# Kernel tuning notes

Measured on AMD Instinct MI355X. Metric: run time of the kernel, lower is better.

The kernel has to match this reference:

```python
import jax, jax.numpy as jnp
import numpy as np

N = 262144
LOC_ENC_LEN = 60
NUM_WEIGHTS = 8
INDIM = 32
OUTDIM = 32
HIDDEN = 32
NEG_SLOPE = 0.01  # nn.LeakyReLU default


def _linear_init(key, fan_in, fan_out):
    # torch nn.Linear default: U(-1/sqrt(fan_in), 1/sqrt(fan_in))
    kw, kb = jax.random.split(key)
    bound = 1.0 / np.sqrt(fan_in)
    w = jax.random.uniform(kw, (fan_in, fan_out), jnp.float32, -bound, bound)
    b = jax.random.uniform(kb, (fan_out,), jnp.float32, -bound, bound)
    return w, b


def setup_inputs() -> dict:
    key = jax.random.key(0)
    ks = jax.random.split(key, 10)
    rel_loc_feat = jax.random.normal(ks[0], (N, LOC_ENC_LEN), jnp.float32)
    feat = jax.random.normal(ks[1], (N, INDIM), jnp.float32)
    dims = [LOC_ENC_LEN, HIDDEN, HIDDEN, HIDDEN, HIDDEN, HIDDEN, NUM_WEIGHTS]
    params = {}
    for i in range(6):
        w, b = _linear_init(ks[2 + i], dims[i], dims[i + 1])
        params[f'sn_w{i}'] = w
        params[f'sn_b{i}'] = b
    # weights_bank: kaiming_normal on [num_weights, indim*outdim] -> std = sqrt(2/fan_in), fan_in = indim*outdim
    std = np.sqrt(2.0 / (INDIM * OUTDIM))
    params['bank'] = jax.random.normal(ks[9], (NUM_WEIGHTS, INDIM * OUTDIM), jnp.float32) * std
    return {'rel_loc_feat': rel_loc_feat, 'feat': feat, **params}


def _score_net(x, ws, bs):
    # 5 Linear+LeakyReLU blocks, then final Linear (no activation)
    for i in range(5):
        x = x @ ws[i] + bs[i]
        x = jnp.where(x >= 0, x, NEG_SLOPE * x)
    return x @ ws[5] + bs[5]


def reference(rel_loc_feat, feat,
              sn_w0, sn_b0, sn_w1, sn_b1, sn_w2, sn_b2,
              sn_w3, sn_b3, sn_w4, sn_b4, sn_w5, sn_b5, bank):
    ws = [sn_w0, sn_w1, sn_w2, sn_w3, sn_w4, sn_w5]
    bs = [sn_b0, sn_b1, sn_b2, sn_b3, sn_b4, sn_b5]
    logits = _score_net(rel_loc_feat, ws, bs)          # [N, num_weights]
    coeff = jax.nn.softmax(logits, axis=-1)            # [N, num_weights]
    # per-point weight matrix: [N, indim*outdim] -> [N, indim, outdim]
    weights = (coeff @ bank).reshape(coeff.shape[0], INDIM, OUTDIM)
    # per-point matmul: feat[:, None] @ weights -> squeeze
    out = jnp.einsum('ni,nio->no', feat, weights)      # [N, outdim]
    return out
```

## Files before the change

### kernel.cpp

```cpp
#include <hip/hip_runtime.h>
#include <stdint.h>


typedef __attribute__((ext_vector_type(8))) __bf16 bf16x8;
typedef __attribute__((ext_vector_type(2))) __bf16 bf16x2;
typedef __attribute__((ext_vector_type(4))) float f32x4;

union FragU { uint32_t u[4]; bf16x8 v; uint4 q; };

__device__ __forceinline__ unsigned short f2bf(float f) {
    union { float f; uint32_t i; } v; v.f = f;
    return (unsigned short)((v.i + 0x7FFFu + ((v.i >> 16) & 1u)) >> 16);
}
__device__ __forceinline__ float bf2f(uint32_t u16) {
    union { uint32_t i; float f; } v; v.i = u16 << 16; return v.f;
}
__device__ __forceinline__ uint32_t pk2(float x, float y) {
    union { bf16x2 h; uint32_t u; } c;
    c.h[0] = (__bf16)x; c.h[1] = (__bf16)y;
    return c.u;
}
__device__ __forceinline__ bf16x8 pack8(float a, float b, float c, float d,
                                        float e, float f, float g, float h) {
    bf16x8 v;
    v[0] = (__bf16)a; v[1] = (__bf16)b; v[2] = (__bf16)c; v[3] = (__bf16)d;
    v[4] = (__bf16)e; v[5] = (__bf16)f; v[6] = (__bf16)g; v[7] = (__bf16)h;
    return v;
}
__device__ __forceinline__ int permK(int k) {
    return 4 * (k >> 3) + (k & 3) + 16 * ((k >> 2) & 1);
}
__device__ __forceinline__ f32x4 MF(bf16x8 a, bf16x8 b, f32x4 c) {
    return __builtin_amdgcn_mfma_f32_16x16x32_bf16(a, b, c, 0, 0, 0);
}


struct WPf { const float* p[13]; };

__global__ void pc_prep(WPf wp, uint32_t* __restrict__ ws) {
    int idx = blockIdx.x * blockDim.x + threadIdx.x;
    if (idx >= 10240) return;
    if (idx < 7424) {
        int layer, t, chunk = 0, lane, d; const float* w; bool perm;
        int r = idx;
        if (r < 1024) { chunk = r >> 9; r &= 511; t = r >> 8; r &= 255; lane = r >> 2; d = r & 3;
                        layer = 0; w = wp.p[0]; perm = false; }
        else if (r < 3072) { r -= 1024; layer = 1 + (r >> 9); r &= 511; t = r >> 8; r &= 255;
                             lane = r >> 2; d = r & 3; w = wp.p[2 * layer]; perm = true; }
        else if (r < 3328) { r -= 3072; layer = 5; t = 0; lane = r >> 2; d = r & 3;
                             w = wp.p[10]; perm = true; }
        else { r -= 3328; int bk = r >> 9; r &= 511; t = r >> 8; r &= 255; lane = r >> 2; d = r & 3;
               layer = -1; w = wp.p[12] + bk * 1024; perm = false; }
        int gq = lane >> 4, m = t * 16 + (lane & 15);
        uint32_t o = 0;
        #pragma unroll
        for (int e = 0; e < 2; ++e) {
            int kf = 8 * gq + 2 * d + e;
            float v = 0.f;
            if (layer == -1) {
                v = w[kf * 32 + m];
            } else {
                int ks = perm ? permK(kf) : (chunk * 32 + kf);
                if (layer == 0)      { if (ks < 60) v = w[ks * 32 + m]; }
                else if (layer == 5) { if (m < 8)   v = w[ks * 8 + m]; }
                else                 v = w[ks * 32 + m];
            }
            o |= ((uint32_t)f2bf(v)) << (16 * e);
        }
        ws[idx] = o;
    } else if (idx < 9984) {
        int r = idx - 7424; int L = r >> 9; r &= 511; int t = r >> 8; r &= 255;
        int lane = r >> 2, rr = r & 3;
        ((float*)ws)[idx] = wp.p[2 * L + 1][t * 16 + 4 * (lane >> 4) + rr];
    } else {
        int r = idx - 9984; int lane = r >> 2, rr = r & 3;
        int m = 4 * (lane >> 4) + rr;
        ((float*)ws)[idx] = (m < 8) ? wp.p[11][m] : 0.f;
    }
}

#define IT 2

__global__ __launch_bounds__(256, 2) void pc_main(
    const float* __restrict__ rel, const float* __restrict__ feat,
    const uint32_t* __restrict__ wsu, float* __restrict__ out)
{
    __shared__ __align__(16) uint32_t W[10240];
    {
        uint4* s4 = (uint4*)W;
        const uint4* g4 = (const uint4*)wsu;
        #pragma unroll
        for (int i = 0; i < 10; ++i) s4[threadIdx.x + 256 * i] = g4[threadIdx.x + 256 * i];
    }
    __syncthreads();

    const int lane = threadIdx.x & 63;
    const int wv = threadIdx.x >> 6;
    const int g = lane >> 4;
    const int n16 = lane & 15;

    f32x4 Bi[5][2], Bi5;
    #pragma unroll
    for (int L = 0; L < 5; ++L)
        #pragma unroll
        for (int t = 0; t < 2; ++t) {
            float4 b = ((const float4*)(W + 7424 + L * 512 + t * 256))[lane];
            Bi[L][t][0] = b.x; Bi[L][t][1] = b.y; Bi[L][t][2] = b.z; Bi[L][t][3] = b.w;
        }
    {
        float4 b = ((const float4*)(W + 9984))[lane];
        Bi5[0] = b.x; Bi5[1] = b.y; Bi5[2] = b.z; Bi5[3] = b.w;
    }

    const size_t pt0 = (size_t)(blockIdx.x * 4 + wv) * (32 * IT);

    #define LDF(off) ({ FragU _f; _f.q = ((const uint4*)(W + (off)))[lane]; _f.v; })

    for (int it = 0; it < IT; ++it) {
        const size_t nA = pt0 + (size_t)it * 32 + n16;

        bf16x8 c0[2], c1[2];
        #pragma unroll
        for (int q = 0; q < 2; ++q) {
            const float* rrow = rel + (nA + 16 * q) * 60;
            float4 ra = *(const float4*)(rrow + 8 * g);
            float4 rb = *(const float4*)(rrow + 8 * g + 4);
            float4 rc = *(const float4*)(rrow + 32 + 8 * g);
            float4 rd = make_float4(0.f, 0.f, 0.f, 0.f);
            if (g < 3) rd = *(const float4*)(rrow + 36 + 8 * g);
            c0[q] = pack8(ra.x, ra.y, ra.z, ra.w, rb.x, rb.y, rb.z, rb.w);
            c1[q] = pack8(rc.x, rc.y, rc.z, rc.w, rd.x, rd.y, rd.z, rd.w);
        }

        f32x4 t0[2], t1[2];
        #pragma unroll
        for (int q = 0; q < 2; ++q) { t0[q] = Bi[0][0]; t1[q] = Bi[0][1]; }
        {
            bf16x8 w00 = LDF(0), w01 = LDF(256), w10 = LDF(512), w11 = LDF(768);
            #pragma unroll
            for (int q = 0; q < 2; ++q) {
                t0[q] = MF(w00, c0[q], t0[q]); t1[q] = MF(w01, c0[q], t1[q]);
                t0[q] = MF(w10, c1[q], t0[q]); t1[q] = MF(w11, c1[q], t1[q]);
            }
        }

        #pragma unroll
        for (int L = 0; L < 4; ++L) {
            bf16x8 wa = LDF(1024 + L * 512), wb = LDF(1024 + L * 512 + 256);
            #pragma unroll
            for (int q = 0; q < 2; ++q) {
                #pragma unroll
                for (int r = 0; r < 4; ++r) {
                    t0[q][r] = fmaxf(t0[q][r], 0.01f * t0[q][r]);
                    t1[q][r] = fmaxf(t1[q][r], 0.01f * t1[q][r]);
                }
                bf16x8 bx = pack8(t0[q][0], t0[q][1], t0[q][2], t0[q][3],
                                  t1[q][0], t1[q][1], t1[q][2], t1[q][3]);
                t0[q] = MF(wa, bx, Bi[L + 1][0]);
                t1[q] = MF(wb, bx, Bi[L + 1][1]);
            }
        }

        {
            bf16x8 w5 = LDF(3072);
            #pragma unroll
            for (int q = 0; q < 2; ++q) {
                #pragma unroll
                for (int r = 0; r < 4; ++r) {
                    t0[q][r] = fmaxf(t0[q][r], 0.01f * t0[q][r]);
                    t1[q][r] = fmaxf(t1[q][r], 0.01f * t1[q][r]);
                }
                bf16x8 bx = pack8(t0[q][0], t0[q][1], t0[q][2], t0[q][3],
                                  t1[q][0], t1[q][1], t1[q][2], t1[q][3]);
                t0[q] = MF(w5, bx, Bi5);
            }
        }

        float cw[2][8];
        #pragma unroll
        for (int q = 0; q < 2; ++q) {
            float m4 = fmaxf(fmaxf(t0[q][0], t0[q][1]), fmaxf(t0[q][2], t0[q][3]));
            float m8 = fmaxf(m4, __shfl_xor(m4, 16, 64));
            float e0 = __expf(t0[q][0] - m8), e1 = __expf(t0[q][1] - m8);
            float e2 = __expf(t0[q][2] - m8), e3 = __expf(t0[q][3] - m8);
            float s4 = e0 + e1 + e2 + e3;
            float s8 = s4 + __shfl_xor(s4, 16, 64);
            float inv = 1.0f / s8;
            uint32_t p01 = pk2(e0 * inv, e1 * inv);
            uint32_t p23 = pk2(e2 * inv, e3 * inv);
            uint32_t q01 = (uint32_t)__builtin_amdgcn_ds_bpermute(n16 * 4, (int)p01);
            uint32_t q23 = (uint32_t)__builtin_amdgcn_ds_bpermute(n16 * 4, (int)p23);
            uint32_t q45 = (uint32_t)__builtin_amdgcn_ds_bpermute((n16 + 16) * 4, (int)p01);
            uint32_t q67 = (uint32_t)__builtin_amdgcn_ds_bpermute((n16 + 16) * 4, (int)p23);
            cw[q][0] = bf2f(q01 & 0xffff); cw[q][1] = bf2f(q01 >> 16);
            cw[q][2] = bf2f(q23 & 0xffff); cw[q][3] = bf2f(q23 >> 16);
            cw[q][4] = bf2f(q45 & 0xffff); cw[q][5] = bf2f(q45 >> 16);
            cw[q][6] = bf2f(q67 & 0xffff); cw[q][7] = bf2f(q67 >> 16);
        }

        bf16x8 bf_[2];
        #pragma unroll
        for (int q = 0; q < 2; ++q) {
            const float* frow = feat + (nA + 16 * q) * 32 + 8 * g;
            float4 fa = *(const float4*)frow;
            float4 fb = *(const float4*)(frow + 4);
            bf_[q] = pack8(fa.x, fa.y, fa.z, fa.w, fb.x, fb.y, fb.z, fb.w);
        }
        f32x4 o0[2], o1[2];
        #pragma unroll
        for (int q = 0; q < 2; ++q) {
            o0[q] = (f32x4){0.f, 0.f, 0.f, 0.f};
            o1[q] = (f32x4){0.f, 0.f, 0.f, 0.f};
        }
        #pragma unroll
        for (int k = 0; k < 8; ++k) {
            bf16x8 wk0 = LDF(3328 + k * 512), wk1 = LDF(3328 + k * 512 + 256);
            #pragma unroll
            for (int q = 0; q < 2; ++q) {
                f32x4 z = {0.f, 0.f, 0.f, 0.f};
                f32x4 u0 = MF(wk0, bf_[q], z);
                f32x4 u1 = MF(wk1, bf_[q], z);
                #pragma unroll
                for (int r = 0; r < 4; ++r) {
                    o0[q][r] += cw[q][k] * u0[r];
                    o1[q][r] += cw[q][k] * u1[r];
                }
            }
        }

        #pragma unroll
        for (int q = 0; q < 2; ++q) {
            float* orow = out + (nA + 16 * q) * 32;
            *(float4*)(orow + 4 * g)      = make_float4(o0[q][0], o0[q][1], o0[q][2], o0[q][3]);
            *(float4*)(orow + 16 + 4 * g) = make_float4(o1[q][0], o1[q][1], o1[q][2], o1[q][3]);
        }
    }
    #undef LDF
}

extern "C" void kernel_launch(void* const* d_in, const int* in_sizes, int n_in,
                              void* d_out, int out_size, void* d_ws, size_t ws_size,
                              hipStream_t stream)
{
    const float* rel = (const float*)d_in[0];
    const float* feat = (const float*)d_in[1];
    WPf wp;
    for (int i = 0; i < 13; ++i) wp.p[i] = (const float*)d_in[2 + i];
    uint32_t* ws = (uint32_t*)d_ws;
    float* out = (float*)d_out;

    const int npts = in_sizes[0] / 60;
    const int nblocks = npts / (32 * IT * 4);

    hipLaunchKernelGGL(pc_prep, dim3(40), dim3(256), 0, stream, wp, ws);
    hipLaunchKernelGGL(pc_main, dim3(nblocks), dim3(256), 0, stream, rel, feat, ws, out);
}
```

Measured before the change: 158.0 us.

## Split fused kernel into MLP+softmax kernel and weight-bank kernel via output buffer

```diff
diff --git a/kernel.cpp b/kernel.cpp
--- a/kernel.cpp
+++ b/kernel.cpp
@@ -81,16 +81,19 @@
 
 #define IT 2
 
-__global__ __launch_bounds__(256, 2) void pc_main(
-    const float* __restrict__ rel, const float* __restrict__ feat,
-    const uint32_t* __restrict__ wsu, float* __restrict__ out)
+__global__ __launch_bounds__(256) void pc_mlp(
+    const float* __restrict__ rel, const uint32_t* __restrict__ wsu,
+    uint32_t* __restrict__ outc)
 {
-    __shared__ __align__(16) uint32_t W[10240];
+    __shared__ __align__(16) uint32_t W[6144];
     {
         uint4* s4 = (uint4*)W;
         const uint4* g4 = (const uint4*)wsu;
         #pragma unroll
-        for (int i = 0; i < 10; ++i) s4[threadIdx.x + 256 * i] = g4[threadIdx.x + 256 * i];
+        for (int i = 0; i < 6; ++i) {
+            int idx = threadIdx.x + 256 * i;
+            s4[idx] = g4[idx < 832 ? idx : idx + 1024];
+        }
     }
     __syncthreads();
 
@@ -98,23 +101,11 @@
     const int wv = threadIdx.x >> 6;
     const int g = lane >> 4;
     const int n16 = lane & 15;
-
-    f32x4 Bi[5][2], Bi5;
-    #pragma unroll
-    for (int L = 0; L < 5; ++L)
-        #pragma unroll
-        for (int t = 0; t < 2; ++t) {
-            float4 b = ((const float4*)(W + 7424 + L * 512 + t * 256))[lane];
-            Bi[L][t][0] = b.x; Bi[L][t][1] = b.y; Bi[L][t][2] = b.z; Bi[L][t][3] = b.w;
-        }
-    {
-        float4 b = ((const float4*)(W + 9984))[lane];
-        Bi5[0] = b.x; Bi5[1] = b.y; Bi5[2] = b.z; Bi5[3] = b.w;
-    }
-
     const size_t pt0 = (size_t)(blockIdx.x * 4 + wv) * (32 * IT);
 
     #define LDF(off) ({ FragU _f; _f.q = ((const uint4*)(W + (off)))[lane]; _f.v; })
+    #define LDB(off) ({ float4 _b = ((const float4*)(W + (off)))[lane]; \
+                        (f32x4){_b.x, _b.y, _b.z, _b.w}; })
 
     for (int it = 0; it < IT; ++it) {
         const size_t nA = pt0 + (size_t)it * 32 + n16;
@@ -133,13 +124,12 @@
         }
 
         f32x4 t0[2], t1[2];
-        #pragma unroll
-        for (int q = 0; q < 2; ++q) { t0[q] = Bi[0][0]; t1[q] = Bi[0][1]; }
         {
+            f32x4 ba = LDB(3328), bb = LDB(3328 + 256);
             bf16x8 w00 = LDF(0), w01 = LDF(256), w10 = LDF(512), w11 = LDF(768);
             #pragma unroll
             for (int q = 0; q < 2; ++q) {
-                t0[q] = MF(w00, c0[q], t0[q]); t1[q] = MF(w01, c0[q], t1[q]);
+                t0[q] = MF(w00, c0[q], ba); t1[q] = MF(w01, c0[q], bb);
                 t0[q] = MF(w10, c1[q], t0[q]); t1[q] = MF(w11, c1[q], t1[q]);
             }
         }
@@ -147,6 +137,7 @@
         #pragma unroll
         for (int L = 0; L < 4; ++L) {
             bf16x8 wa = LDF(1024 + L * 512), wb = LDF(1024 + L * 512 + 256);
+            f32x4 ba = LDB(3328 + (L + 1) * 512), bb = LDB(3328 + (L + 1) * 512 + 256);
             #pragma unroll
             for (int q = 0; q < 2; ++q) {
                 #pragma unroll
@@ -156,13 +147,14 @@
                 }
                 bf16x8 bx = pack8(t0[q][0], t0[q][1], t0[q][2], t0[q][3],
                                   t1[q][0], t1[q][1], t1[q][2], t1[q][3]);
-                t0[q] = MF(wa, bx, Bi[L + 1][0]);
-                t1[q] = MF(wb, bx, Bi[L + 1][1]);
+                t0[q] = MF(wa, bx, ba);
+                t1[q] = MF(wb, bx, bb);
             }
         }
 
         {
             bf16x8 w5 = LDF(3072);
+            f32x4 b5 = LDB(5888);
             #pragma unroll
             for (int q = 0; q < 2; ++q) {
                 #pragma unroll
@@ -172,11 +164,10 @@
                 }
                 bf16x8 bx = pack8(t0[q][0], t0[q][1], t0[q][2], t0[q][3],
                                   t1[q][0], t1[q][1], t1[q][2], t1[q][3]);
-                t0[q] = MF(w5, bx, Bi5);
-            }
-        }
-
-        float cw[2][8];
+                t0[q] = MF(w5, bx, b5);
+            }
+        }
+
         #pragma unroll
         for (int q = 0; q < 2; ++q) {
             float m4 = fmaxf(fmaxf(t0[q][0], t0[q][1]), fmaxf(t0[q][2], t0[q][3]));
@@ -188,24 +179,62 @@
             float inv = 1.0f / s8;
             uint32_t p01 = pk2(e0 * inv, e1 * inv);
             uint32_t p23 = pk2(e2 * inv, e3 * inv);
-            uint32_t q01 = (uint32_t)__builtin_amdgcn_ds_bpermute(n16 * 4, (int)p01);
-            uint32_t q23 = (uint32_t)__builtin_amdgcn_ds_bpermute(n16 * 4, (int)p23);
-            uint32_t q45 = (uint32_t)__builtin_amdgcn_ds_bpermute((n16 + 16) * 4, (int)p01);
-            uint32_t q67 = (uint32_t)__builtin_amdgcn_ds_bpermute((n16 + 16) * 4, (int)p23);
-            cw[q][0] = bf2f(q01 & 0xffff); cw[q][1] = bf2f(q01 >> 16);
-            cw[q][2] = bf2f(q23 & 0xffff); cw[q][3] = bf2f(q23 >> 16);
-            cw[q][4] = bf2f(q45 & 0xffff); cw[q][5] = bf2f(q45 >> 16);
-            cw[q][6] = bf2f(q67 & 0xffff); cw[q][7] = bf2f(q67 >> 16);
-        }
-
-        bf16x8 bf_[2];
+            if (g < 2)
+                *(uint2*)(outc + (nA + 16 * q) * 32 + 2 * g) = make_uint2(p01, p23);
+        }
+    }
+    #undef LDF
+    #undef LDB
+}
+
+__global__ __launch_bounds__(256) void pc_bank(
+    const float* __restrict__ feat, const uint32_t* __restrict__ wsu,
+    float* out)
+{
+    __shared__ __align__(16) uint32_t W[4096];
+    {
+        uint4* s4 = (uint4*)W;
+        const uint4* g4 = (const uint4*)wsu + 832;
+        #pragma unroll
+        for (int i = 0; i < 4; ++i) s4[threadIdx.x + 256 * i] = g4[threadIdx.x + 256 * i];
+    }
+    __syncthreads();
+
+    const uint32_t* outc = (const uint32_t*)out;
+    const int lane = threadIdx.x & 63;
+    const int wv = threadIdx.x >> 6;
+    const int g = lane >> 4;
+    const int n16 = lane & 15;
+    const size_t pt0 = (size_t)(blockIdx.x * 4 + wv) * (32 * IT);
+
+    #define LDF(off) ({ FragU _f; _f.q = ((const uint4*)(W + (off)))[lane]; _f.v; })
+
+    for (int it = 0; it < IT; ++it) {
+        const size_t nA = pt0 + (size_t)it * 32 + n16;
+
+        uint4 cp[2];
+        #pragma unroll
+        for (int q = 0; q < 2; ++q)
+            cp[q] = *(const uint4*)(outc + (nA + 16 * q) * 32);
+
+        bf16x8 bfr[2];
         #pragma unroll
         for (int q = 0; q < 2; ++q) {
             const float* frow = feat + (nA + 16 * q) * 32 + 8 * g;
             float4 fa = *(const float4*)frow;
             float4 fb = *(const float4*)(frow + 4);
-            bf_[q] = pack8(fa.x, fa.y, fa.z, fa.w, fb.x, fb.y, fb.z, fb.w);
-        }
+            bfr[q] = pack8(fa.x, fa.y, fa.z, fa.w, fb.x, fb.y, fb.z, fb.w);
+        }
+
+        float cw[2][8];
+        #pragma unroll
+        for (int q = 0; q < 2; ++q) {
+            cw[q][0] = bf2f(cp[q].x & 0xffff); cw[q][1] = bf2f(cp[q].x >> 16);
+            cw[q][2] = bf2f(cp[q].y & 0xffff); cw[q][3] = bf2f(cp[q].y >> 16);
+            cw[q][4] = bf2f(cp[q].z & 0xffff); cw[q][5] = bf2f(cp[q].z >> 16);
+            cw[q][6] = bf2f(cp[q].w & 0xffff); cw[q][7] = bf2f(cp[q].w >> 16);
+        }
+
         f32x4 o0[2], o1[2];
         #pragma unroll
         for (int q = 0; q < 2; ++q) {
@@ -214,12 +243,12 @@
         }
         #pragma unroll
         for (int k = 0; k < 8; ++k) {
-            bf16x8 wk0 = LDF(3328 + k * 512), wk1 = LDF(3328 + k * 512 + 256);
+            bf16x8 wk0 = LDF(k * 512), wk1 = LDF(k * 512 + 256);
             #pragma unroll
             for (int q = 0; q < 2; ++q) {
                 f32x4 z = {0.f, 0.f, 0.f, 0.f};
-                f32x4 u0 = MF(wk0, bf_[q], z);
-                f32x4 u1 = MF(wk1, bf_[q], z);
+                f32x4 u0 = MF(wk0, bfr[q], z);
+                f32x4 u1 = MF(wk1, bfr[q], z);
                 #pragma unroll
                 for (int r = 0; r < 4; ++r) {
                     o0[q][r] += cw[q][k] * u0[r];
@@ -253,5 +282,6 @@
     const int nblocks = npts / (32 * IT * 4);
 
     hipLaunchKernelGGL(pc_prep, dim3(40), dim3(256), 0, stream, wp, ws);
-    hipLaunchKernelGGL(pc_main, dim3(nblocks), dim3(256), 0, stream, rel, feat, ws, out);
-}
+    hipLaunchKernelGGL(pc_mlp, dim3(nblocks), dim3(256), 0, stream, rel, ws, (uint32_t*)out);
+    hipLaunchKernelGGL(pc_bank, dim3(nblocks), dim3(256), 0, stream, feat, ws, out);
+}
```

After: 180.5 us. 1.14x slower.
